# Kernel tuning notes

Hardware: AMD Instinct MI355X
Metric: run time of the kernel (lower is better)

## Reference

```python
import jax, jax.numpy as jnp
import numpy as np

N_QUBITS = 10
QLCU_LAYERS = 2
FEATURE_DIM = 256
BATCH = 256
N_PARAMS = 5 * N_QUBITS * QLCU_LAYERS  # 100
TWO_PI = 2.0 * np.pi


def _rx_mat(theta):
    # (B,) -> (B,2,2) complex64
    c = jnp.cos(theta / 2).astype(jnp.complex64)
    s = (-1j * jnp.sin(theta / 2)).astype(jnp.complex64)
    return jnp.stack([jnp.stack([c, s], -1), jnp.stack([s, c], -1)], -2)


def _ry_mat(theta):
    c = jnp.cos(theta / 2).astype(jnp.complex64)
    s = jnp.sin(theta / 2).astype(jnp.complex64)
    return jnp.stack([jnp.stack([c, -s], -1), jnp.stack([s, c], -1)], -2)


def _rz_mat(theta):
    e0 = jnp.exp(-0.5j * theta.astype(jnp.complex64))
    e1 = jnp.exp(0.5j * theta.astype(jnp.complex64))
    z = jnp.zeros_like(e0)
    return jnp.stack([jnp.stack([e0, z], -1), jnp.stack([z, e1], -1)], -2)


def _apply_1q(state, U, w):
    # state: (B,)+(2,)*n ; U: (B,2,2) ; wire w (PennyLane wire 0 = most significant)
    s = jnp.moveaxis(state, 1 + w, -1)
    s = jnp.einsum('bij,b...j->b...i', U, s)
    return jnp.moveaxis(s, -1, 1 + w)


def _apply_crx(state, theta, c, t):
    # controlled-RX: apply RX(theta) on target t where control c == 1
    s = jnp.moveaxis(state, (1 + c, 1 + t), (-2, -1))
    U = _rx_mat(theta)
    s1 = jnp.einsum('bij,b...j->b...i', U, s[..., 1, :])
    s = jnp.stack([s[..., 0, :], s1], axis=-2)
    return jnp.moveaxis(s, (-2, -1), (1 + c, 1 + t))


def _circuit(params):
    # params: (B, N_PARAMS) angles. Returns (B, 3*n) expvals [X.., Y.., Z..]
    n = N_QUBITS
    B = params.shape[0]
    state = jnp.zeros((B,) + (2,) * n, jnp.complex64)
    state = state.at[(slice(None),) + (0,) * n].set(1.0)
    idx = 0
    for _ in range(QLCU_LAYERS):
        for i in range(n):
            state = _apply_1q(state, _rx_mat(params[:, idx]), i)
            state = _apply_1q(state, _ry_mat(params[:, idx + 1]), i)
            state = _apply_1q(state, _rz_mat(params[:, idx + 2]), i)
            idx += 3
        for i in range(n):
            state = _apply_crx(state, params[:, idx], i, (i + 1) % n)
            idx += 1
        for i in range(n - 1, -1, -1):
            state = _apply_crx(state, params[:, idx], i, (i - 1) % n)
            idx += 1
    X, Y, Z = [], [], []
    for w in range(n):
        s = jnp.moveaxis(state, 1 + w, -1).reshape(B, -1, 2)
        z01 = jnp.sum(jnp.conj(s[..., 0]) * s[..., 1], axis=1)  # (B,)
        X.append(2.0 * jnp.real(z01))
        Y.append(2.0 * jnp.imag(z01))
        probs = jnp.sum(jnp.abs(s) ** 2, axis=1)  # (B,2)
        Z.append(probs[:, 0] - probs[:, 1])
    return jnp.stack(X + Y + Z, axis=1).astype(jnp.float32)


def _branch(x, W, b, base):
    p = x @ W.T + b            # (B, N_PARAMS)
    p = p + base[None, :]
    p = jax.nn.sigmoid(p) * TWO_PI
    return _circuit(p)


def setup_inputs() -> dict:
    key = jax.random.key(0)
    ks = jax.random.split(key, 16)
    d = {
        'x': jax.random.normal(ks[0], (BATCH, FEATURE_DIM), jnp.float32),
        'W1': jax.random.normal(ks[1], (N_PARAMS, FEATURE_DIM), jnp.float32) * 0.05,
        'b1': jnp.zeros((N_PARAMS,), jnp.float32),
        'W2': jax.random.normal(ks[2], (N_PARAMS, FEATURE_DIM), jnp.float32) * 0.05,
        'b2': jnp.zeros((N_PARAMS,), jnp.float32),
        'W3': jax.random.normal(ks[3], (N_PARAMS, FEATURE_DIM), jnp.float32) * 0.05,
        'b3': jnp.zeros((N_PARAMS,), jnp.float32),
        'base1': jax.random.uniform(ks[4], (N_PARAMS,), jnp.float32) * TWO_PI,
        'base2': jax.random.uniform(ks[5], (N_PARAMS,), jnp.float32) * TWO_PI,
        'base3': jax.random.uniform(ks[6], (N_PARAMS,), jnp.float32) * TWO_PI,
        'alpha_real': jax.random.uniform(ks[7], (1,), jnp.float32),
        'alpha_imag': jnp.zeros((1,), jnp.float32),
        'beta_real': jax.random.uniform(ks[8], (1,), jnp.float32),
        'beta_imag': jnp.zeros((1,), jnp.float32),
        'gamma_real': jax.random.uniform(ks[9], (1,), jnp.float32),
        'gamma_imag': jnp.zeros((1,), jnp.float32),
    }
    return d


def reference(x, W1, b1, W2, b2, W3, b3, base1, base2, base3,
              alpha_real, alpha_imag, beta_real, beta_imag, gamma_real, gamma_imag):
    m1 = _branch(x, W1, b1, base1)  # (B, 3n)
    m2 = _branch(x, W2, b2, base2)
    m3 = _branch(x, W3, b3, base3)
    norm = jnp.sqrt(alpha_real**2 + alpha_imag**2 + beta_real**2 + beta_imag**2
                    + gamma_real**2 + gamma_imag**2 + 1e-9)
    ar, ai = alpha_real / norm, alpha_imag / norm
    br, bi = beta_real / norm, beta_imag / norm
    gr, gi = gamma_real / norm, gamma_imag / norm
    re = ar * m1 + br * m2 + gr * m3
    im = ai * m1 + bi * m2 + gi * m3
    return jnp.sqrt(re * re + im * im)
```

## Files before the change

### kernel.cpp

```cpp
#include <hip/hip_runtime.h>
#include <math.h>

#define NQ 10
#define NPAR 100
#define FDIM 256
#define BATCH 256
#define NOUT 30
#define TWO_PI_F 6.283185307179586f


__device__ __forceinline__ float shx(float v, int mask) {
    return __shfl_xor(v, mask, 64);
}

template<int BIT>
__device__ __forceinline__ void gate1q(float2 (&st)[16], int lane,
                                       float2 u00, float2 u01, float2 u10, float2 u11)
{
    if constexpr (BIT >= 6) {
        constexpr int rb = 1 << (BIT - 6);
        #pragma unroll
        for (int a = 0; a < 16; ++a) {
            if (a & rb) continue;
            const int a1 = a | rb;
            const float2 A0 = st[a], A1 = st[a1];
            float2 n0, n1;
            n0.x = u00.x*A0.x - u00.y*A0.y + u01.x*A1.x - u01.y*A1.y;
            n0.y = u00.x*A0.y + u00.y*A0.x + u01.x*A1.y + u01.y*A1.x;
            n1.x = u10.x*A0.x - u10.y*A0.y + u11.x*A1.x - u11.y*A1.y;
            n1.y = u10.x*A0.y + u10.y*A0.x + u11.x*A1.y + u11.y*A1.x;
            st[a] = n0; st[a1] = n1;
        }
    } else {
        constexpr int lb = 1 << BIT;
        const bool hi = (lane & lb) != 0;
        const float2 A = hi ? u11 : u00;
        const float2 B = hi ? u10 : u01;
        #pragma unroll
        for (int a = 0; a < 16; ++a) {
            const float2 m = st[a];
            float2 p;
            p.x = shx(m.x, lb); p.y = shx(m.y, lb);
            float2 n;
            n.x = A.x*m.x - A.y*m.y + B.x*p.x - B.y*p.y;
            n.y = A.x*m.y + A.y*m.x + B.x*p.y + B.y*p.x;
            st[a] = n;
        }
    }
}

template<int BC, int BT>
__device__ __forceinline__ void crx(float2 (&st)[16], int lane, float c, float s)
{
    if constexpr (BT >= 6) {
        constexpr int rt = 1 << (BT - 6);
        if constexpr (BC >= 6) {
            constexpr int rc = 1 << (BC - 6);
            #pragma unroll
            for (int a = 0; a < 16; ++a) {
                if (!(a & rc) || (a & rt)) continue;
                const int a1 = a | rt;
                const float2 A0 = st[a], A1 = st[a1];
                float2 n0, n1;
                n0.x = c*A0.x + s*A1.y;  n0.y = c*A0.y - s*A1.x;
                n1.x = c*A1.x + s*A0.y;  n1.y = c*A1.y - s*A0.x;
                st[a] = n0; st[a1] = n1;
            }
        } else {
            constexpr int lc = 1 << BC;
            const bool act = (lane & lc) != 0;
            const float cc = act ? c : 1.f;
            const float ss = act ? s : 0.f;
            #pragma unroll
            for (int a = 0; a < 16; ++a) {
                if (a & rt) continue;
                const int a1 = a | rt;
                const float2 A0 = st[a], A1 = st[a1];
                float2 n0, n1;
                n0.x = cc*A0.x + ss*A1.y;  n0.y = cc*A0.y - ss*A1.x;
                n1.x = cc*A1.x + ss*A0.y;  n1.y = cc*A1.y - ss*A0.x;
                st[a] = n0; st[a1] = n1;
            }
        }
    } else {
        constexpr int lt = 1 << BT;
        float cc, ss;
        if constexpr (BC < 6) {
            constexpr int lc = 1 << BC;
            const bool act = (lane & lc) != 0;
            cc = act ? c : 1.f;
            ss = act ? s : 0.f;
        } else { cc = c; ss = s; }
        #pragma unroll
        for (int a = 0; a < 16; ++a) {
            if constexpr (BC >= 6) {
                constexpr int rc = 1 << (BC - 6);
                if (!(a & rc)) continue;
            }
            const float2 m = st[a];
            float2 p;
            p.x = shx(m.x, lt); p.y = shx(m.y, lt);
            float2 n;
            n.x = cc*m.x + ss*p.y;
            n.y = cc*m.y - ss*p.x;
            st[a] = n;
        }
    }
}

template<int Q>
__device__ __forceinline__ void layer1q(float2 (&st)[16], int lane, const float2* cs, int idx)
{
    if constexpr (Q < NQ) {
        const float2 X = cs[idx], Y = cs[idx + 1], Z = cs[idx + 2];
        const float cx = X.x, sx = X.y, cy = Y.x, sy = Y.y, cz = Z.x, sz = Z.y;
        const float2 m00 = make_float2( cy*cx,  sy*sx);
        const float2 m01 = make_float2(-sy*cx, -cy*sx);
        const float2 m10 = make_float2( sy*cx, -cy*sx);
        const float2 m11 = make_float2( cy*cx, -sy*sx);
        const float2 u00 = make_float2(cz*m00.x + sz*m00.y, cz*m00.y - sz*m00.x);
        const float2 u01 = make_float2(cz*m01.x + sz*m01.y, cz*m01.y - sz*m01.x);
        const float2 u10 = make_float2(cz*m10.x - sz*m10.y, cz*m10.y + sz*m10.x);
        const float2 u11 = make_float2(cz*m11.x - sz*m11.y, cz*m11.y + sz*m11.x);
        gate1q<9 - Q>(st, lane, u00, u01, u10, u11);
        layer1q<Q + 1>(st, lane, cs, idx + 3);
    }
}

template<int Q>
__device__ __forceinline__ void ringF(float2 (&st)[16], int lane, const float2* cs, int idx)
{
    if constexpr (Q < NQ) {
        const float2 p = cs[idx];
        crx<9 - Q, 9 - ((Q + 1) % NQ)>(st, lane, p.x, p.y);
        ringF<Q + 1>(st, lane, cs, idx + 1);
    }
}

template<int Q>
__device__ __forceinline__ void ringB(float2 (&st)[16], int lane, const float2* cs, int idx)
{
    if constexpr (Q >= 0) {
        const float2 p = cs[idx];
        crx<9 - Q, 9 - ((Q + NQ - 1) % NQ)>(st, lane, p.x, p.y);
        ringB<Q - 1>(st, lane, cs, idx + 1);
    }
}

template<int W>
__device__ __forceinline__ void measureAll(const float2 (&st)[16], int lane, float* m_row)
{
    if constexpr (W < NQ) {
        constexpr int B = 9 - W;
        float sre = 0.f, smm = 0.f, szz = 0.f;
        if constexpr (B >= 6) {
            constexpr int rb = 1 << (B - 6);
            #pragma unroll
            for (int a = 0; a < 16; ++a) {
                if (a & rb) continue;
                const int a1 = a | rb;
                const float2 A0 = st[a], A1 = st[a1];
                sre += A0.x*A1.x + A0.y*A1.y;
                smm += A0.x*A1.y - A0.y*A1.x;
                szz += A0.x*A0.x + A0.y*A0.y - A1.x*A1.x - A1.y*A1.y;
            }
            sre *= 2.f; smm *= 2.f;
        } else {
            constexpr int lb = 1 << B;
            const float sgn = (lane & lb) ? -1.f : 1.f;
            #pragma unroll
            for (int a = 0; a < 16; ++a) {
                const float2 m = st[a];
                float2 p;
                p.x = shx(m.x, lb); p.y = shx(m.y, lb);
                sre += m.x*p.x + m.y*p.y;
                smm += sgn * (m.x*p.y - m.y*p.x);
                szz += sgn * (m.x*m.x + m.y*m.y - p.x*p.x - p.y*p.y);
            }
            szz *= 0.5f;
        }
        #pragma unroll
        for (int off = 1; off < 64; off <<= 1) {
            sre += shx(sre, off);
            smm += shx(smm, off);
            szz += shx(szz, off);
        }
        if (lane == 0) {
            m_row[W]      = sre;
            m_row[10 + W] = smm;
            m_row[20 + W] = szz;
        }
        measureAll<W + 1>(st, lane, m_row);
    }
}

__global__ __launch_bounds__(64) void qsb_branch(
    const float* __restrict__ x,
    const float* __restrict__ W1, const float* __restrict__ b1, const float* __restrict__ base1,
    const float* __restrict__ W2, const float* __restrict__ b2, const float* __restrict__ base2,
    const float* __restrict__ W3, const float* __restrict__ b3, const float* __restrict__ base3,
    float* __restrict__ m_ws)
{
    const int sim  = blockIdx.x;
    const int b    = sim & (BATCH - 1);
    const int br   = sim >> 8;
    const int lane = threadIdx.x;

    const float* W    = (br == 0) ? W1    : (br == 1) ? W2    : W3;
    const float* bias = (br == 0) ? b1    : (br == 1) ? b2    : b3;
    const float* base = (br == 0) ? base1 : (br == 1) ? base2 : base3;

    __shared__ float2 cs[NPAR];

    if (lane < 50) {
        const int p0 = 2 * lane;
        const float4* xr = reinterpret_cast<const float4*>(x + (size_t)b * FDIM);
        const float4* w0 = reinterpret_cast<const float4*>(W + (size_t)p0 * FDIM);
        const float4* w1 = reinterpret_cast<const float4*>(W + (size_t)(p0 + 1) * FDIM);
        float acc0 = 0.f, acc1 = 0.f;
        #pragma unroll 8
        for (int k = 0; k < FDIM / 4; ++k) {
            const float4 xv = xr[k];
            const float4 a  = w0[k];
            const float4 bb = w1[k];
            acc0 += xv.x*a.x  + xv.y*a.y  + xv.z*a.z  + xv.w*a.w;
            acc1 += xv.x*bb.x + xv.y*bb.y + xv.z*bb.z + xv.w*bb.w;
        }
        acc0 += bias[p0]     + base[p0];
        acc1 += bias[p0 + 1] + base[p0 + 1];
        const float t0 = TWO_PI_F / (1.f + __expf(-acc0));
        const float t1 = TWO_PI_F / (1.f + __expf(-acc1));
        float s0, c0, s1, c1;
        __sincosf(0.5f * t0, &s0, &c0);
        __sincosf(0.5f * t1, &s1, &c1);
        cs[p0]     = make_float2(c0, s0);
        cs[p0 + 1] = make_float2(c1, s1);
    }
    __syncthreads();

    float2 st[16];
    #pragma unroll
    for (int a = 0; a < 16; ++a) st[a] = make_float2(0.f, 0.f);
    if (lane == 0) st[0].x = 1.f;

    layer1q<0>(st, lane, cs, 0);
    ringF<0>(st, lane, cs, 30);
    ringB<NQ - 1>(st, lane, cs, 40);
    layer1q<0>(st, lane, cs, 50);
    ringF<0>(st, lane, cs, 80);
    ringB<NQ - 1>(st, lane, cs, 90);

    float* m_row = m_ws + ((size_t)br * BATCH + b) * NOUT;
    measureAll<0>(st, lane, m_row);
}

__global__ __launch_bounds__(256) void qsb_combine(
    const float* __restrict__ m,
    const float* __restrict__ ar_, const float* __restrict__ ai_,
    const float* __restrict__ br_, const float* __restrict__ bi_,
    const float* __restrict__ gr_, const float* __restrict__ gi_,
    float* __restrict__ out)
{
    const int i = blockIdx.x * blockDim.x + threadIdx.x;
    if (i >= BATCH * NOUT) return;
    const float ar = ar_[0], ai = ai_[0];
    const float br = br_[0], bi = bi_[0];
    const float gr = gr_[0], gi = gi_[0];
    const float inv = 1.f / sqrtf(ar*ar + ai*ai + br*br + bi*bi + gr*gr + gi*gi + 1e-9f);
    const float m1 = m[i];
    const float m2 = m[BATCH * NOUT + i];
    const float m3 = m[2 * BATCH * NOUT + i];
    const float re = (ar * m1 + br * m2 + gr * m3) * inv;
    const float im = (ai * m1 + bi * m2 + gi * m3) * inv;
    out[i] = sqrtf(re * re + im * im);
}

extern "C" void kernel_launch(void* const* d_in, const int* in_sizes, int n_in,
                              void* d_out, int out_size, void* d_ws, size_t ws_size,
                              hipStream_t stream)
{
    (void)in_sizes; (void)n_in; (void)out_size; (void)ws_size;
    const float* x     = (const float*)d_in[0];
    const float* W1    = (const float*)d_in[1];
    const float* b1    = (const float*)d_in[2];
    const float* W2    = (const float*)d_in[3];
    const float* b2    = (const float*)d_in[4];
    const float* W3    = (const float*)d_in[5];
    const float* b3    = (const float*)d_in[6];
    const float* base1 = (const float*)d_in[7];
    const float* base2 = (const float*)d_in[8];
    const float* base3 = (const float*)d_in[9];
    const float* ar    = (const float*)d_in[10];
    const float* ai    = (const float*)d_in[11];
    const float* br    = (const float*)d_in[12];
    const float* bi    = (const float*)d_in[13];
    const float* gr    = (const float*)d_in[14];
    const float* gi    = (const float*)d_in[15];

    float* m_ws = (float*)d_ws;
    float* out  = (float*)d_out;

    qsb_branch<<<dim3(BATCH * 3), dim3(64), 0, stream>>>(
        x, W1, b1, base1, W2, b2, base2, W3, b3, base3, m_ws);
    qsb_combine<<<(BATCH * NOUT + 255) / 256, 256, 0, stream>>>(
        m_ws, ar, ai, br, bi, gr, gi, out);
}
```

Before: 125.7 us.

## Build initial product state analytically and batch shuffles and reductions

The first layer of single-qubit rotations on |0…0> is replaced by a closed-form product state built from the first column of each combined rotation, which removes ten gate applications and their cross-lane shuffles. Shuffles inside the gate, CRX and measurement loops are issued for all 16 amplitudes up front so they can overlap instead of alternating with arithmetic. The ten per-wire butterfly reductions are interleaved into one loop and written out in a single store pass, and the matvec unroll factor is raised. In exchange the code holds more live registers (a 16-entry partner array plus 30 partial sums), which may raise VGPR pressure.

```diff
diff --git a/kernel.cpp b/kernel.cpp
--- a/kernel.cpp
+++ b/kernel.cpp
@@ -11,6 +11,10 @@
 
 __device__ __forceinline__ float shx(float v, int mask) {
     return __shfl_xor(v, mask, 64);
+}
+
+__device__ __forceinline__ float2 cmul(float2 a, float2 b) {
+    return make_float2(a.x*b.x - a.y*b.y, a.x*b.y + a.y*b.x);
 }
 
 template<int BIT>
@@ -33,17 +37,21 @@
         }
     } else {
         constexpr int lb = 1 << BIT;
+        float2 p[16];
+        #pragma unroll
+        for (int a = 0; a < 16; ++a) {
+            p[a].x = shx(st[a].x, lb);
+            p[a].y = shx(st[a].y, lb);
+        }
         const bool hi = (lane & lb) != 0;
         const float2 A = hi ? u11 : u00;
         const float2 B = hi ? u10 : u01;
         #pragma unroll
         for (int a = 0; a < 16; ++a) {
             const float2 m = st[a];
-            float2 p;
-            p.x = shx(m.x, lb); p.y = shx(m.y, lb);
             float2 n;
-            n.x = A.x*m.x - A.y*m.y + B.x*p.x - B.y*p.y;
-            n.y = A.x*m.y + A.y*m.x + B.x*p.y + B.y*p.x;
+            n.x = A.x*m.x - A.y*m.y + B.x*p[a].x - B.y*p[a].y;
+            n.y = A.x*m.y + A.y*m.x + B.x*p[a].y + B.y*p[a].x;
             st[a] = n;
         }
     }
@@ -91,18 +99,19 @@
             cc = act ? c : 1.f;
             ss = act ? s : 0.f;
         } else { cc = c; ss = s; }
-        #pragma unroll
-        for (int a = 0; a < 16; ++a) {
-            if constexpr (BC >= 6) {
-                constexpr int rc = 1 << (BC - 6);
-                if (!(a & rc)) continue;
-            }
-            const float2 m = st[a];
-            float2 p;
-            p.x = shx(m.x, lt); p.y = shx(m.y, lt);
+        float2 p[16];
+        #pragma unroll
+        for (int a = 0; a < 16; ++a) {
+            if constexpr (BC >= 6) { if (!(a & (1 << (BC - 6)))) continue; }
+            p[a].x = shx(st[a].x, lt);
+            p[a].y = shx(st[a].y, lt);
+        }
+        #pragma unroll
+        for (int a = 0; a < 16; ++a) {
+            if constexpr (BC >= 6) { if (!(a & (1 << (BC - 6)))) continue; }
             float2 n;
-            n.x = cc*m.x + ss*p.y;
-            n.y = cc*m.y - ss*p.x;
+            n.x = cc*st[a].x + ss*p[a].y;
+            n.y = cc*st[a].y - ss*p[a].x;
             st[a] = n;
         }
     }
@@ -147,8 +156,19 @@
     }
 }
 
+__device__ __forceinline__ void col0(const float2* cs, int w, float2& u00, float2& u10)
+{
+    const float2 X = cs[3*w], Y = cs[3*w + 1], Z = cs[3*w + 2];
+    const float cx = X.x, sx = X.y, cy = Y.x, sy = Y.y, cz = Z.x, sz = Z.y;
+    const float2 m00 = make_float2(cy*cx,  sy*sx);
+    const float2 m10 = make_float2(sy*cx, -cy*sx);
+    u00 = make_float2(cz*m00.x + sz*m00.y, cz*m00.y - sz*m00.x);
+    u10 = make_float2(cz*m10.x - sz*m10.y, cz*m10.y + sz*m10.x);
+}
+
 template<int W>
-__device__ __forceinline__ void measureAll(const float2 (&st)[16], int lane, float* m_row)
+__device__ __forceinline__ void measurePartials(const float2 (&st)[16], int lane,
+                                                float (&vx)[10], float (&vy)[10], float (&vz)[10])
 {
     if constexpr (W < NQ) {
         constexpr int B = 9 - W;
@@ -167,30 +187,24 @@
             sre *= 2.f; smm *= 2.f;
         } else {
             constexpr int lb = 1 << B;
+            float2 p[16];
+            #pragma unroll
+            for (int a = 0; a < 16; ++a) {
+                p[a].x = shx(st[a].x, lb);
+                p[a].y = shx(st[a].y, lb);
+            }
             const float sgn = (lane & lb) ? -1.f : 1.f;
             #pragma unroll
             for (int a = 0; a < 16; ++a) {
                 const float2 m = st[a];
-                float2 p;
-                p.x = shx(m.x, lb); p.y = shx(m.y, lb);
-                sre += m.x*p.x + m.y*p.y;
-                smm += sgn * (m.x*p.y - m.y*p.x);
-                szz += sgn * (m.x*m.x + m.y*m.y - p.x*p.x - p.y*p.y);
+                sre += m.x*p[a].x + m.y*p[a].y;
+                smm += sgn * (m.x*p[a].y - m.y*p[a].x);
+                szz += sgn * (m.x*m.x + m.y*m.y - p[a].x*p[a].x - p[a].y*p[a].y);
             }
             szz *= 0.5f;
         }
-        #pragma unroll
-        for (int off = 1; off < 64; off <<= 1) {
-            sre += shx(sre, off);
-            smm += shx(smm, off);
-            szz += shx(szz, off);
-        }
-        if (lane == 0) {
-            m_row[W]      = sre;
-            m_row[10 + W] = smm;
-            m_row[20 + W] = szz;
-        }
-        measureAll<W + 1>(st, lane, m_row);
+        vx[W] = sre; vy[W] = smm; vz[W] = szz;
+        measurePartials<W + 1>(st, lane, vx, vy, vz);
     }
 }
 
@@ -218,7 +232,7 @@
         const float4* w0 = reinterpret_cast<const float4*>(W + (size_t)p0 * FDIM);
         const float4* w1 = reinterpret_cast<const float4*>(W + (size_t)(p0 + 1) * FDIM);
         float acc0 = 0.f, acc1 = 0.f;
-        #pragma unroll 8
+        #pragma unroll 16
         for (int k = 0; k < FDIM / 4; ++k) {
             const float4 xv = xr[k];
             const float4 a  = w0[k];
@@ -239,19 +253,56 @@
     __syncthreads();
 
     float2 st[16];
-    #pragma unroll
-    for (int a = 0; a < 16; ++a) st[a] = make_float2(0.f, 0.f);
-    if (lane == 0) st[0].x = 1.f;
-
-    layer1q<0>(st, lane, cs, 0);
+    {
+        float2 lp = make_float2(1.f, 0.f);
+        #pragma unroll
+        for (int bb = 0; bb < 6; ++bb) {
+            float2 u00, u10;
+            col0(cs, 9 - bb, u00, u10);
+            const float2 sel = ((lane >> bb) & 1) ? u10 : u00;
+            lp = cmul(lp, sel);
+        }
+        float2 v3[2], v2[2], v1[2], v0[2];
+        col0(cs, 3, v3[0], v3[1]);
+        col0(cs, 2, v2[0], v2[1]);
+        col0(cs, 1, v1[0], v1[1]);
+        col0(cs, 0, v0[0], v0[1]);
+        #pragma unroll
+        for (int a = 0; a < 16; ++a) {
+            float2 t = cmul(v3[a & 1], v2[(a >> 1) & 1]);
+            t = cmul(t, cmul(v1[(a >> 2) & 1], v0[(a >> 3) & 1]));
+            st[a] = cmul(t, lp);
+        }
+    }
+
     ringF<0>(st, lane, cs, 30);
     ringB<NQ - 1>(st, lane, cs, 40);
     layer1q<0>(st, lane, cs, 50);
     ringF<0>(st, lane, cs, 80);
     ringB<NQ - 1>(st, lane, cs, 90);
 
-    float* m_row = m_ws + ((size_t)br * BATCH + b) * NOUT;
-    measureAll<0>(st, lane, m_row);
+    float vx[10], vy[10], vz[10];
+    measurePartials<0>(st, lane, vx, vy, vz);
+
+    #pragma unroll
+    for (int off = 1; off < 64; off <<= 1) {
+        #pragma unroll
+        for (int w = 0; w < 10; ++w) {
+            vx[w] += shx(vx[w], off);
+            vy[w] += shx(vy[w], off);
+            vz[w] += shx(vz[w], off);
+        }
+    }
+
+    if (lane == 0) {
+        float* m_row = m_ws + ((size_t)br * BATCH + b) * NOUT;
+        #pragma unroll
+        for (int w = 0; w < 10; ++w) {
+            m_row[w]      = vx[w];
+            m_row[10 + w] = vy[w];
+            m_row[20 + w] = vz[w];
+        }
+    }
 }
 
 __global__ __launch_bounds__(256) void qsb_combine(
```

Result: faster. 121.7 us (-3.2%).

## Fuse branch and combine kernels and build first layer as product state analytically

Applied to the files above, without the earlier changes.

Merges the three branch simulations for one batch row into a single 192-thread block. Measurements stay in shared memory and the combine step runs in the same kernel, which removes the second launch and the workspace round trip. The first layer of single-qubit gates acts on |0...0>, so it now builds the resulting product state directly from each qubit's combined first column instead of applying 30 gates. This removes one launch and a large share of gate arithmetic. In exchange there are fewer blocks (256 instead of 768) and higher register pressure per block.

```diff
diff --git a/kernel.cpp b/kernel.cpp
--- a/kernel.cpp
+++ b/kernel.cpp
@@ -11,6 +11,10 @@
 
 __device__ __forceinline__ float shx(float v, int mask) {
     return __shfl_xor(v, mask, 64);
+}
+
+__device__ __forceinline__ float2 cmul(float2 a, float2 b) {
+    return make_float2(a.x*b.x - a.y*b.y, a.x*b.y + a.y*b.x);
 }
 
 template<int BIT>
@@ -147,6 +151,16 @@
     }
 }
 
+__device__ __forceinline__ void col0(const float2* cs, int w, float2& u00, float2& u10)
+{
+    const float2 X = cs[3*w], Y = cs[3*w + 1], Z = cs[3*w + 2];
+    const float cx = X.x, sx = X.y, cy = Y.x, sy = Y.y, cz = Z.x, sz = Z.y;
+    const float2 m00 = make_float2(cy*cx,  sy*sx);
+    const float2 m10 = make_float2(sy*cx, -cy*sx);
+    u00 = make_float2(cz*m00.x + sz*m00.y, cz*m00.y - sz*m00.x);
+    u10 = make_float2(cz*m10.x - sz*m10.y, cz*m10.y + sz*m10.x);
+}
+
 template<int W>
 __device__ __forceinline__ void measureAll(const float2 (&st)[16], int lane, float* m_row)
 {
@@ -194,23 +208,27 @@
     }
 }
 
-__global__ __launch_bounds__(64) void qsb_branch(
+__global__ __launch_bounds__(192) void qsb_fused(
     const float* __restrict__ x,
     const float* __restrict__ W1, const float* __restrict__ b1, const float* __restrict__ base1,
     const float* __restrict__ W2, const float* __restrict__ b2, const float* __restrict__ base2,
     const float* __restrict__ W3, const float* __restrict__ b3, const float* __restrict__ base3,
-    float* __restrict__ m_ws)
-{
-    const int sim  = blockIdx.x;
-    const int b    = sim & (BATCH - 1);
-    const int br   = sim >> 8;
-    const int lane = threadIdx.x;
-
-    const float* W    = (br == 0) ? W1    : (br == 1) ? W2    : W3;
-    const float* bias = (br == 0) ? b1    : (br == 1) ? b2    : b3;
-    const float* base = (br == 0) ? base1 : (br == 1) ? base2 : base3;
-
-    __shared__ float2 cs[NPAR];
+    const float* __restrict__ ar_, const float* __restrict__ ai_,
+    const float* __restrict__ br_, const float* __restrict__ bi_,
+    const float* __restrict__ gr_, const float* __restrict__ gi_,
+    float* __restrict__ out)
+{
+    const int b    = blockIdx.x;
+    const int wv   = threadIdx.x >> 6;
+    const int lane = threadIdx.x & 63;
+
+    const float* W    = (wv == 0) ? W1    : (wv == 1) ? W2    : W3;
+    const float* bias = (wv == 0) ? b1    : (wv == 1) ? b2    : b3;
+    const float* base = (wv == 0) ? base1 : (wv == 1) ? base2 : base3;
+
+    __shared__ float2 css[3][NPAR];
+    __shared__ float  mloc[3][NOUT];
+    float2* cs = css[wv];
 
     if (lane < 50) {
         const int p0 = 2 * lane;
@@ -239,47 +257,56 @@
     __syncthreads();
 
     float2 st[16];
-    #pragma unroll
-    for (int a = 0; a < 16; ++a) st[a] = make_float2(0.f, 0.f);
-    if (lane == 0) st[0].x = 1.f;
-
-    layer1q<0>(st, lane, cs, 0);
+    {
+        float2 lp = make_float2(1.f, 0.f);
+        #pragma unroll
+        for (int bb = 0; bb < 6; ++bb) {
+            float2 u00, u10;
+            col0(cs, 9 - bb, u00, u10);
+            const float2 sel = ((lane >> bb) & 1) ? u10 : u00;
+            lp = cmul(lp, sel);
+        }
+        float2 v3[2], v2[2], v1[2], v0[2];
+        col0(cs, 3, v3[0], v3[1]);
+        col0(cs, 2, v2[0], v2[1]);
+        col0(cs, 1, v1[0], v1[1]);
+        col0(cs, 0, v0[0], v0[1]);
+        #pragma unroll
+        for (int a = 0; a < 16; ++a) {
+            float2 t = cmul(v3[a & 1], v2[(a >> 1) & 1]);
+            t = cmul(t, cmul(v1[(a >> 2) & 1], v0[(a >> 3) & 1]));
+            st[a] = cmul(t, lp);
+        }
+    }
+
     ringF<0>(st, lane, cs, 30);
     ringB<NQ - 1>(st, lane, cs, 40);
     layer1q<0>(st, lane, cs, 50);
     ringF<0>(st, lane, cs, 80);
     ringB<NQ - 1>(st, lane, cs, 90);
 
-    float* m_row = m_ws + ((size_t)br * BATCH + b) * NOUT;
-    measureAll<0>(st, lane, m_row);
-}
-
-__global__ __launch_bounds__(256) void qsb_combine(
-    const float* __restrict__ m,
-    const float* __restrict__ ar_, const float* __restrict__ ai_,
-    const float* __restrict__ br_, const float* __restrict__ bi_,
-    const float* __restrict__ gr_, const float* __restrict__ gi_,
-    float* __restrict__ out)
-{
-    const int i = blockIdx.x * blockDim.x + threadIdx.x;
-    if (i >= BATCH * NOUT) return;
-    const float ar = ar_[0], ai = ai_[0];
-    const float br = br_[0], bi = bi_[0];
-    const float gr = gr_[0], gi = gi_[0];
-    const float inv = 1.f / sqrtf(ar*ar + ai*ai + br*br + bi*bi + gr*gr + gi*gi + 1e-9f);
-    const float m1 = m[i];
-    const float m2 = m[BATCH * NOUT + i];
-    const float m3 = m[2 * BATCH * NOUT + i];
-    const float re = (ar * m1 + br * m2 + gr * m3) * inv;
-    const float im = (ai * m1 + bi * m2 + gi * m3) * inv;
-    out[i] = sqrtf(re * re + im * im);
+    measureAll<0>(st, lane, mloc[wv]);
+    __syncthreads();
+
+    if (threadIdx.x < NOUT) {
+        const int i = threadIdx.x;
+        const float ar = ar_[0], ai = ai_[0];
+        const float br = br_[0], bi = bi_[0];
+        const float gr = gr_[0], gi = gi_[0];
+        const float inv = 1.f / sqrtf(ar*ar + ai*ai + br*br + bi*bi
+                                      + gr*gr + gi*gi + 1e-9f);
+        const float m1 = mloc[0][i], m2 = mloc[1][i], m3 = mloc[2][i];
+        const float re = (ar * m1 + br * m2 + gr * m3) * inv;
+        const float im = (ai * m1 + bi * m2 + gi * m3) * inv;
+        out[(size_t)b * NOUT + i] = sqrtf(re * re + im * im);
+    }
 }
 
 extern "C" void kernel_launch(void* const* d_in, const int* in_sizes, int n_in,
                               void* d_out, int out_size, void* d_ws, size_t ws_size,
                               hipStream_t stream)
 {
-    (void)in_sizes; (void)n_in; (void)out_size; (void)ws_size;
+    (void)in_sizes; (void)n_in; (void)out_size; (void)d_ws; (void)ws_size;
     const float* x     = (const float*)d_in[0];
     const float* W1    = (const float*)d_in[1];
     const float* b1    = (const float*)d_in[2];
@@ -297,11 +324,7 @@
     const float* gr    = (const float*)d_in[14];
     const float* gi    = (const float*)d_in[15];
 
-    float* m_ws = (float*)d_ws;
-    float* out  = (float*)d_out;
-
-    qsb_branch<<<dim3(BATCH * 3), dim3(64), 0, stream>>>(
-        x, W1, b1, base1, W2, b2, base2, W3, b3, base3, m_ws);
-    qsb_combine<<<(BATCH * NOUT + 255) / 256, 256, 0, stream>>>(
-        m_ws, ar, ai, br, bi, gr, gi, out);
-}
+    qsb_fused<<<dim3(BATCH), dim3(192), 0, stream>>>(
+        x, W1, b1, base1, W2, b2, base2, W3, b3, base3,
+        ar, ai, br, bi, gr, gi, (float*)d_out);
+}
```

Result: faster. 117.3 us (-6.7%).
